# Kernel tuning notes

Hardware: AMD Instinct MI355X
Metric: run time of the kernel (lower is better)

The kernel has to match this reference:

```python
import jax, jax.numpy as jnp
import numpy as np

B, C, H, W = 16, 64, 128, 128
MX, MY = 24, 24
HIDDEN = max(1, int(C * 0.5))


def setup_inputs() -> dict:
    key = jax.random.key(0)
    ks = jax.random.split(key, 9)
    scale = 1.0 / (C * C)
    return {
        "x": jax.random.normal(ks[0], (B, C, H, W), jnp.float32),
        "w_real": scale * jax.random.normal(ks[1], (MX, MY, C, C), jnp.float32),
        "w_imag": scale * jax.random.normal(ks[2], (MX, MY, C, C), jnp.float32),
        "w_skip": jax.random.normal(ks[3], (C, C), jnp.float32) * (1.0 / np.sqrt(C)),
        "fc1_w": jax.random.normal(ks[4], (HIDDEN, C), jnp.float32) * (1.0 / np.sqrt(C)),
        "fc1_b": jnp.zeros((HIDDEN,), jnp.float32),
        "fc2_w": jax.random.normal(ks[5], (C, HIDDEN), jnp.float32) * (1.0 / np.sqrt(HIDDEN)),
        "fc2_b": jnp.zeros((C,), jnp.float32),
        "gate": jnp.ones((1, C, 1, 1), jnp.float32),
    }


def _spectral_conv(x, w_real, w_imag):
    # x: (B, C, H, W). Hermitian-symmetric 2-D spectral conv, matching torch path.
    b, c, h, w = x.shape
    mx = min(MX, h)
    my = min(MY, w // 2 + 1)
    x_ft = jnp.fft.rfftn(x, axes=(-2, -1))            # (B, C, H, W//2+1) complex
    weight = (w_real[:mx, :my] + 1j * w_imag[:mx, :my]).astype(jnp.complex64)
    out_sl = jnp.einsum('bcxy,xyco->boxy', x_ft[:, :, :mx, :my], weight)
    out_ft = jnp.zeros((b, c, h, w // 2 + 1), jnp.complex64).at[:, :, :mx, :my].set(out_sl)
    # enforce_hermitian_symmetry=True: ifft over leading spatial dim, zero imag
    # of DC / Nyquist columns, then irfft over last dim.
    out_ft = jnp.fft.ifft(out_ft, n=h, axis=-2)
    out_ft = out_ft.at[..., 0].set(out_ft[..., 0].real.astype(jnp.complex64))
    if w % 2 == 0:
        out_ft = out_ft.at[..., -1].set(out_ft[..., -1].real.astype(jnp.complex64))
    return jnp.fft.irfft(out_ft, n=w, axis=-1)


def reference(x, w_real, w_imag, w_skip, fc1_w, fc1_b, fc2_w, fc2_b, gate):
    # fno skip: 1x1 conv, no bias
    skip = jnp.einsum('bchw,oc->bohw', x, w_skip)
    h1 = jax.nn.gelu(_spectral_conv(x, w_real, w_imag) + skip, approximate=False)
    # channel MLP (Conv1d kernel=1 == per-pixel channel matmul)
    z = jnp.einsum('bchw,kc->bkhw', h1, fc1_w) + fc1_b[None, :, None, None]
    z = jax.nn.gelu(z, approximate=False)
    z = jnp.einsum('bkhw,ck->bchw', z, fc2_w) + fc2_b[None, :, None, None]
    # soft-gating skip
    return z + gate * h1
```

## Files before the change

kernel.cpp:

```cpp
#include <hip/hip_runtime.h>
#include <hip/hip_bf16.h>

#define BF __hip_bfloat16


typedef __attribute__((ext_vector_type(8))) short s8b;
typedef __attribute__((ext_vector_type(4))) float f32x4;

__device__ __forceinline__ float erf_fast(float x) {
    float ax = fabsf(x);
    float t  = 1.0f / (1.0f + 0.3275911f * ax);
    float p  = t * (0.254829592f + t * (-0.284496736f + t * (1.421413741f
             + t * (-1.453152027f + t * 1.061405429f))));
    float r  = 1.0f - p * __expf(-ax * ax);
    return copysignf(r, x);
}
__device__ __forceinline__ float geluf(float v) {
    return 0.5f * v * (1.0f + erf_fast(v * 0.7071067811865476f));
}
__device__ __forceinline__ float bf2f(BF v) { return __bfloat162float(v); }
__device__ __forceinline__ short f2bs(float f) {
    union { BF h; short s; } u; u.h = __float2bfloat16(f); return u.s;
}
__device__ __forceinline__ s8b ld8f(const float* __restrict__ p) {
    float4 a = *(const float4*)p;
    float4 b = *(const float4*)(p + 4);
    s8b r;
    r[0] = f2bs(a.x); r[1] = f2bs(a.y); r[2] = f2bs(a.z); r[3] = f2bs(a.w);
    r[4] = f2bs(b.x); r[5] = f2bs(b.y); r[6] = f2bs(b.z); r[7] = f2bs(b.w);
    return r;
}

__global__ __launch_bounds__(256) void k_tw(BF* __restrict__ gB1,
                                            BF* __restrict__ gB2) {
    int idx = blockIdx.x * 256 + threadIdx.x;
    if (idx < 6144) {
        int y = idx >> 7, v = idx & 127;
        int yy = (y < 24) ? y : y - 24;
        int r = (v * yy) & 127;
        float s, c; __sincosf((float)r * 0.04908738521234052f, &s, &c);
        gB1[idx] = __float2bfloat16(y < 24 ? c : -s);
    } else {
        int j = idx - 6144;
        int xp = j >> 8, k = j & 255;
        int u = k & 127, half = k >> 7;
        int x = (xp < 24) ? xp : xp - 24;
        int r = (u * x) & 127;
        float s, c; __sincosf((float)r * 0.04908738521234052f, &s, &c);
        float val = (xp < 24) ? (half ? s : c) : (half ? c : -s);
        gB2[j] = __float2bfloat16(val);
    }
}

__global__ __launch_bounds__(256) void k_fwd(const float* __restrict__ x,
                                             const BF* __restrict__ gB1,
                                             const BF* __restrict__ gB2,
                                             BF* __restrict__ XrB,
                                             BF* __restrict__ XiB) {
    __shared__ __align__(16) short Tl[48 * 136];

    const int tid  = threadIdx.x;
    const int bc   = blockIdx.x;
    const int lane = tid & 63;
    const int wv   = tid >> 6;
    const int lr   = lane & 15;
    const int lg   = lane >> 4;

    {
        const float* xb = x + ((size_t)bc << 14);
        s8b af[2][4];
        #pragma unroll
        for (int m = 0; m < 2; ++m) {
            const int u = wv * 32 + m * 16 + lr;
            #pragma unroll
            for (int s = 0; s < 4; ++s)
                af[m][s] = ld8f(xb + (size_t)u * 128 + s * 32 + lg * 8);
        }
        f32x4 acc[2][3];
        #pragma unroll
        for (int m = 0; m < 2; ++m)
            #pragma unroll
            for (int n = 0; n < 3; ++n)
                #pragma unroll
                for (int r = 0; r < 4; ++r) acc[m][n][r] = 0.f;
        #pragma unroll
        for (int s = 0; s < 4; ++s)
            #pragma unroll
            for (int n = 0; n < 3; ++n) {
                s8b bfr = *(const s8b*)((const short*)gB1 + (n * 16 + lr) * 128 + s * 32 + lg * 8);
                #pragma unroll
                for (int m = 0; m < 2; ++m)
                    acc[m][n] = __builtin_amdgcn_mfma_f32_16x16x32_bf16(af[m][s], bfr, acc[m][n], 0, 0, 0);
            }
        #pragma unroll
        for (int m = 0; m < 2; ++m) {
            const int u0 = wv * 32 + m * 16 + lg * 4;
            #pragma unroll
            for (int n = 0; n < 3; ++n) {
                short4 t;
                t.x = f2bs(acc[m][n][0]); t.y = f2bs(acc[m][n][1]);
                t.z = f2bs(acc[m][n][2]); t.w = f2bs(acc[m][n][3]);
                *(short4*)&Tl[(n * 16 + lr) * 136 + u0] = t;
            }
        }
    }
    __syncthreads();

    for (int j = wv; j < 6; j += 4) {
        const int m = j / 3, n = j % 3;
        const int y  = m * 16 + lr;
        const int r1 = (y < 24) ? y      : 0;
        const int r2 = (y < 24) ? y + 24 : 0;
        f32x4 acc = {0.f, 0.f, 0.f, 0.f};
        #pragma unroll
        for (int s = 0; s < 8; ++s) {
            s8b a = *(const s8b*)&Tl[((s < 4) ? r1 : r2) * 136 + (s & 3) * 32 + lg * 8];
            s8b b = *(const s8b*)((const short*)gB2 + (n * 16 + lr) * 256 + s * 32 + lg * 8);
            acc = __builtin_amdgcn_mfma_f32_16x16x32_bf16(a, b, acc, 0, 0, 0);
        }
        const int col = n * 16 + lr;
        const int xc  = (col < 24) ? col : col - 24;
        BF* dst = (col < 24) ? XrB : XiB;
        #pragma unroll
        for (int r = 0; r < 4; ++r) {
            const int yo = m * 16 + lg * 4 + r;
            if (yo < 24)
                dst[(size_t)(xc * 24 + yo) * 1024 + bc] = __float2bfloat16(acc[r]);
        }
    }
}

__global__ __launch_bounds__(256) void k_mix(const float* __restrict__ wr_g,
                                             const float* __restrict__ wi_g,
                                             const BF* __restrict__ XrB,
                                             const BF* __restrict__ XiB,
                                             BF* __restrict__ SrB,
                                             BF* __restrict__ SiB) {
    __shared__ __align__(16) short Br[64 * 136], Bi[64 * 136];
    const int tid  = threadIdx.x;
    const int xy   = blockIdx.x;
    const int lane = tid & 63;
    const int wv   = tid >> 6;
    const int lr   = lane & 15;
    const int lg   = lane >> 4;

    const float* wrp = wr_g + ((size_t)xy << 12);
    const float* wip = wi_g + ((size_t)xy << 12);
    for (int i = tid; i < 4096; i += 256) {
        int c = i >> 6, o = i & 63;
        float vr = wrp[i], vi = wip[i];
        short br = f2bs(vr), bi = f2bs(vi), nbi = f2bs(-vi);
        Br[o * 136 + c]      = br;
        Br[o * 136 + 64 + c] = nbi;
        Bi[o * 136 + c]      = bi;
        Bi[o * 136 + 64 + c] = br;
    }

    s8b az[4];
    {
        const short* xr = (const short*)XrB + ((size_t)xy << 10) + lr * 64;
        const short* xi = (const short*)XiB + ((size_t)xy << 10) + lr * 64;
        #pragma unroll
        for (int s = 0; s < 2; ++s) {
            az[s]     = *(const s8b*)(xr + s * 32 + lg * 8);
            az[s + 2] = *(const s8b*)(xi + s * 32 + lg * 8);
        }
    }
    __syncthreads();

    f32x4 ar = {0.f, 0.f, 0.f, 0.f}, ai = {0.f, 0.f, 0.f, 0.f};
    #pragma unroll
    for (int s = 0; s < 4; ++s) {
        s8b brf = *(const s8b*)&Br[(wv * 16 + lr) * 136 + s * 32 + lg * 8];
        ar = __builtin_amdgcn_mfma_f32_16x16x32_bf16(az[s], brf, ar, 0, 0, 0);
    }
    #pragma unroll
    for (int s = 0; s < 4; ++s) {
        s8b bif = *(const s8b*)&Bi[(wv * 16 + lr) * 136 + s * 32 + lg * 8];
        ai = __builtin_amdgcn_mfma_f32_16x16x32_bf16(az[s], bif, ai, 0, 0, 0);
    }

    const int o = wv * 16 + lr;
    #pragma unroll
    for (int r = 0; r < 4; ++r) {
        int b = lg * 4 + r;
        size_t base = (size_t)((b << 6) + o) * 576 + xy;
        SrB[base] = __float2bfloat16(ar[r]);
        SiB[base] = __float2bfloat16(ai[r]);
    }
}

__global__ __launch_bounds__(256) void k_invP(const BF* __restrict__ SrB,
                                              const BF* __restrict__ SiB,
                                              BF* __restrict__ PrB,
                                              BF* __restrict__ PiB) {
    __shared__ __align__(16) short Bp[48 * 72];
    const int tid  = threadIdx.x;
    const int bo   = blockIdx.x;
    const int lane = tid & 63;
    const int wv   = tid >> 6;
    const int lr   = lane & 15;
    const int lg   = lane >> 4;
    const float inv = 6.103515625e-05f;

    for (int i = tid; i < 576; i += 256) {
        int x = i / 24, y = i - x * 24;
        float sr = bf2f(SrB[(size_t)bo * 576 + i]);
        float si = bf2f(SiB[(size_t)bo * 576 + i]);
        float sc = (y == 0) ? inv : 2.0f * inv;
        Bp[y * 72 + x]             = f2bs(sc * sr);
        Bp[y * 72 + 24 + x]        = f2bs(-sc * si);
        Bp[(24 + y) * 72 + x]      = f2bs((y == 0) ? 0.f : sc * si);
        Bp[(24 + y) * 72 + 24 + x] = f2bs((y == 0) ? 0.f : sc * sr);
    }
    for (int i = tid; i < 768; i += 256)
        Bp[(i >> 4) * 72 + 48 + (i & 15)] = 0;

    s8b a[2][2];
    #pragma unroll
    for (int m = 0; m < 2; ++m) {
        const int u = wv * 32 + m * 16 + lr;
        #pragma unroll
        for (int s = 0; s < 2; ++s) {
            #pragma unroll
            for (int j = 0; j < 8; ++j) {
                const int k = s * 32 + lg * 8 + j;
                float val = 0.f;
                if (k < 48) {
                    int x = (k < 24) ? k : k - 24;
                    int r = (u * x) & 127;
                    float sn, cs;
                    __sincosf((float)r * 0.04908738521234052f, &sn, &cs);
                    val = (k < 24) ? cs : sn;
                }
                a[m][s][j] = f2bs(val);
            }
        }
    }
    __syncthreads();

    #pragma unroll
    for (int m = 0; m < 2; ++m)
        #pragma unroll
        for (int n = 0; n < 3; ++n) {
            f32x4 acc = {0.f, 0.f, 0.f, 0.f};
            #pragma unroll
            for (int s = 0; s < 2; ++s) {
                s8b bfr = *(const s8b*)&Bp[(n * 16 + lr) * 72 + s * 32 + lg * 8];
                acc = __builtin_amdgcn_mfma_f32_16x16x32_bf16(a[m][s], bfr, acc, 0, 0, 0);
            }
            const int col = n * 16 + lr;
            BF* dst = (col < 24) ? PrB : PiB;
            const int y = (col < 24) ? col : col - 24;
            #pragma unroll
            for (int r = 0; r < 4; ++r) {
                const int u = wv * 32 + m * 16 + lg * 4 + r;
                dst[(size_t)bo * 3072 + (size_t)u * 24 + y] = __float2bfloat16(acc[r]);
            }
        }
}

__global__ __launch_bounds__(256) void k_fused(const float* __restrict__ x,
                                               const BF* __restrict__ PrB,
                                               const BF* __restrict__ PiB,
                                               const float* __restrict__ wsk,
                                               const float* __restrict__ w1,
                                               const float* __restrict__ b1,
                                               const float* __restrict__ w2,
                                               const float* __restrict__ b2,
                                               const float* __restrict__ gt,
                                               float* __restrict__ out) {
    __shared__ __align__(16) short Plds[64 * 72];
    __shared__ __align__(16) short H1s[128 * 72];
    __shared__ __align__(16) short Zls[128 * 40];

    const int tid  = threadIdx.x;
    const int b    = blockIdx.x >> 7;
    const int u    = blockIdx.x & 127;
    const int lane = tid & 63;
    const int wv   = tid >> 6;
    const int lr   = lane & 15;
    const int lg   = lane >> 4;
    const int vb   = wv * 32;

    {
        const size_t pb = (size_t)(b * 64) * 3072 + (size_t)u * 24;
        for (int i = tid; i < 1536; i += 256) {
            int o = i / 24, y = i - o * 24;
            size_t g = pb + (size_t)o * 3072 + y;
            Plds[o * 72 + y]      = *(const short*)&PrB[g];
            Plds[o * 72 + 24 + y] = *(const short*)&PiB[g];
        }
        for (int i = tid; i < 1024; i += 256)
            Plds[(i >> 4) * 72 + 48 + (i & 15)] = 0;
    }

    s8b bx[2][2];
    {
        const float* xb = x + (size_t)(b * 64) * 16384 + (size_t)u * 128;
        #pragma unroll
        for (int nv = 0; nv < 2; ++nv) {
            const int v = vb + nv * 16 + lr;
            #pragma unroll
            for (int s = 0; s < 2; ++s)
                #pragma unroll
                for (int j = 0; j < 8; ++j)
                    bx[nv][s][j] = f2bs(xb[(size_t)(s * 32 + lg * 8 + j) * 16384 + v]);
        }
    }

    s8b btw[2][2];
    #pragma unroll
    for (int nv = 0; nv < 2; ++nv) {
        const int v = vb + nv * 16 + lr;
        #pragma unroll
        for (int s = 0; s < 2; ++s) {
            #pragma unroll
            for (int j = 0; j < 8; ++j) {
                const int k = s * 32 + lg * 8 + j;
                float val = 0.f;
                if (k < 24) {
                    int r = (v * k) & 127;
                    val = __cosf((float)r * 0.04908738521234052f);
                } else if (k < 48) {
                    int r = (v * (k - 24)) & 127;
                    val = -__sinf((float)r * 0.04908738521234052f);
                }
                btw[nv][s][j] = f2bs(val);
            }
        }
    }
    __syncthreads();

    f32x4 acc[4][2];
    #pragma unroll
    for (int mo = 0; mo < 4; ++mo)
        #pragma unroll
        for (int nv = 0; nv < 2; ++nv)
            #pragma unroll
            for (int r = 0; r < 4; ++r) acc[mo][nv][r] = 0.f;

    #pragma unroll
    for (int s = 0; s < 2; ++s)
        #pragma unroll
        for (int mo = 0; mo < 4; ++mo) {
            s8b ap = *(const s8b*)&Plds[(mo * 16 + lr) * 72 + s * 32 + lg * 8];
            #pragma unroll
            for (int nv = 0; nv < 2; ++nv)
                acc[mo][nv] = __builtin_amdgcn_mfma_f32_16x16x32_bf16(ap, btw[nv][s], acc[mo][nv], 0, 0, 0);
        }
    #pragma unroll
    for (int s = 0; s < 2; ++s)
        #pragma unroll
        for (int mo = 0; mo < 4; ++mo) {
            s8b aw = ld8f(wsk + (mo * 16 + lr) * 64 + s * 32 + lg * 8);
            #pragma unroll
            for (int nv = 0; nv < 2; ++nv)
                acc[mo][nv] = __builtin_amdgcn_mfma_f32_16x16x32_bf16(aw, bx[nv][s], acc[mo][nv], 0, 0, 0);
        }

    f32x4 h1r[4][2];
    #pragma unroll
    for (int mo = 0; mo < 4; ++mo)
        #pragma unroll
        for (int nv = 0; nv < 2; ++nv)
            #pragma unroll
            for (int r = 0; r < 4; ++r) {
                float h = geluf(acc[mo][nv][r]);
                h1r[mo][nv][r] = h;
                H1s[(vb + nv * 16 + lr) * 72 + mo * 16 + lg * 4 + r] = f2bs(h);
            }
    __syncthreads();

    f32x4 zac[2][2];
    #pragma unroll
    for (int mk = 0; mk < 2; ++mk)
        #pragma unroll
        for (int nv = 0; nv < 2; ++nv)
            #pragma unroll
            for (int r = 0; r < 4; ++r) zac[mk][nv][r] = 0.f;
    #pragma unroll
    for (int s = 0; s < 2; ++s) {
        s8b bh[2];
        #pragma unroll
        for (int nv = 0; nv < 2; ++nv)
            bh[nv] = *(const s8b*)&H1s[(vb + nv * 16 + lr) * 72 + s * 32 + lg * 8];
        #pragma unroll
        for (int mk = 0; mk < 2; ++mk) {
            s8b aw = ld8f(w1 + (mk * 16 + lr) * 64 + s * 32 + lg * 8);
            #pragma unroll
            for (int nv = 0; nv < 2; ++nv)
                zac[mk][nv] = __builtin_amdgcn_mfma_f32_16x16x32_bf16(aw, bh[nv], zac[mk][nv], 0, 0, 0);
        }
    }
    #pragma unroll
    for (int mk = 0; mk < 2; ++mk)
        #pragma unroll
        for (int r = 0; r < 4; ++r) {
            const float bb = b1[mk * 16 + lg * 4 + r];
            #pragma unroll
            for (int nv = 0; nv < 2; ++nv)
                Zls[(vb + nv * 16 + lr) * 40 + mk * 16 + lg * 4 + r] =
                    f2bs(geluf(zac[mk][nv][r] + bb));
        }
    __syncthreads();

    f32x4 oac[4][2];
    #pragma unroll
    for (int mo = 0; mo < 4; ++mo)
        #pragma unroll
        for (int nv = 0; nv < 2; ++nv)
            #pragma unroll
            for (int r = 0; r < 4; ++r) oac[mo][nv][r] = 0.f;
    s8b bz[2];
    #pragma unroll
    for (int nv = 0; nv < 2; ++nv)
        bz[nv] = *(const s8b*)&Zls[(vb + nv * 16 + lr) * 40 + lg * 8];
    #pragma unroll
    for (int mo = 0; mo < 4; ++mo) {
        s8b aw = ld8f(w2 + (mo * 16 + lr) * 32 + lg * 8);
        #pragma unroll
        for (int nv = 0; nv < 2; ++nv)
            oac[mo][nv] = __builtin_amdgcn_mfma_f32_16x16x32_bf16(aw, bz[nv], oac[mo][nv], 0, 0, 0);
    }

    float* ob = out + (size_t)(b * 64) * 16384 + (size_t)u * 128;
    #pragma unroll
    for (int mo = 0; mo < 4; ++mo)
        #pragma unroll
        for (int r = 0; r < 4; ++r) {
            const int o = mo * 16 + lg * 4 + r;
            const float b2v = b2[o];
            const float gv  = gt[o];
            #pragma unroll
            for (int nv = 0; nv < 2; ++nv)
                ob[(size_t)o * 16384 + vb + nv * 16 + lr] =
                    oac[mo][nv][r] + b2v + gv * h1r[mo][nv][r];
        }
}

extern "C" void kernel_launch(void* const* d_in, const int* in_sizes, int n_in,
                              void* d_out, int out_size, void* d_ws, size_t ws_size,
                              hipStream_t stream) {
    (void)in_sizes; (void)n_in; (void)out_size; (void)ws_size;
    const float* x   = (const float*)d_in[0];
    const float* wr  = (const float*)d_in[1];
    const float* wi  = (const float*)d_in[2];
    const float* wsk = (const float*)d_in[3];
    const float* w1  = (const float*)d_in[4];
    const float* b1  = (const float*)d_in[5];
    const float* w2  = (const float*)d_in[6];
    const float* b2  = (const float*)d_in[7];
    const float* gt  = (const float*)d_in[8];

    BF* wsB = (BF*)d_ws;
    BF* gB1 = wsB;
    BF* gB2 = wsB + 6144;
    BF* Xr  = wsB + 6291456;
    BF* Xi  = wsB + 6881280;
    BF* Sr  = wsB;
    BF* Si  = wsB + 589824;
    BF* Pr  = wsB + 1179648;
    BF* Pi  = wsB + 4325376;

    hipLaunchKernelGGL(k_tw,   dim3(72),   dim3(256), 0, stream, gB1, gB2);
    hipLaunchKernelGGL(k_fwd,  dim3(1024), dim3(256), 0, stream, x, gB1, gB2, Xr, Xi);
    hipLaunchKernelGGL(k_mix,  dim3(576),  dim3(256), 0, stream, wr, wi, Xr, Xi, Sr, Si);
    hipLaunchKernelGGL(k_invP, dim3(1024), dim3(256), 0, stream, Sr, Si, Pr, Pi);
    hipLaunchKernelGGL(k_fused, dim3(2048), dim3(256), 0, stream,
                       x, Pr, Pi, wsk, w1, b1, w2, b2, gt, (float*)d_out);
}
```

Before: 222.9 us.

## Precompute twiddle tables and bf16 weights once, shrink mix LDS and Pi storage

The setup kernel now also builds bf16 twiddle tables for the inverse-P and fused stages and converts the skip and MLP weights to bf16 once. k_invP and k_fused load these tables from memory instead of running sincos per lane, and load packed bf16 weights instead of converting fp32 on the fly. k_mix stores only the real and imaginary weights in half-size LDS and gets the negated term by flipping the sign bit of the activations. The always-zero first imaginary column of P is no longer stored, which cuts intermediate traffic. The cost is more workspace and extra global loads of the tables.

```diff
diff --git a/kernel.cpp b/kernel.cpp
--- a/kernel.cpp
+++ b/kernel.cpp
@@ -31,24 +31,56 @@
     return r;
 }
 
-__global__ __launch_bounds__(256) void k_tw(BF* __restrict__ gB1,
-                                            BF* __restrict__ gB2) {
-    int idx = blockIdx.x * 256 + threadIdx.x;
+__global__ __launch_bounds__(256) void k_tw(const float* __restrict__ wsk,
+                                            const float* __restrict__ w1,
+                                            const float* __restrict__ w2,
+                                            BF* __restrict__ gB1,
+                                            BF* __restrict__ gB2,
+                                            BF* __restrict__ gTw,
+                                            BF* __restrict__ gTa,
+                                            BF* __restrict__ wkB,
+                                            BF* __restrict__ w1B,
+                                            BF* __restrict__ w2B) {
+    const int idx = blockIdx.x * 256 + threadIdx.x;
+    const float th = 0.04908738521234052f;
     if (idx < 6144) {
         int y = idx >> 7, v = idx & 127;
         int yy = (y < 24) ? y : y - 24;
         int r = (v * yy) & 127;
-        float s, c; __sincosf((float)r * 0.04908738521234052f, &s, &c);
+        float s, c; __sincosf((float)r * th, &s, &c);
         gB1[idx] = __float2bfloat16(y < 24 ? c : -s);
-    } else {
+    } else if (idx < 18432) {
         int j = idx - 6144;
         int xp = j >> 8, k = j & 255;
         int u = k & 127, half = k >> 7;
         int x = (xp < 24) ? xp : xp - 24;
         int r = (u * x) & 127;
-        float s, c; __sincosf((float)r * 0.04908738521234052f, &s, &c);
+        float s, c; __sincosf((float)r * th, &s, &c);
         float val = (xp < 24) ? (half ? s : c) : (half ? c : -s);
         gB2[j] = __float2bfloat16(val);
+    } else if (idx < 26624) {
+        int j = idx - 18432;
+        int v = j >> 6, k = j & 63;
+        float val = 0.f;
+        if (k < 24)      val =  __cosf((float)((v * k) & 127) * th);
+        else if (k < 48) val = -__sinf((float)((v * (k - 24)) & 127) * th);
+        gTw[j] = __float2bfloat16(val);
+    } else if (idx < 34816) {
+        int j = idx - 26624;
+        int u = j >> 6, k = j & 63;
+        float val = 0.f;
+        if (k < 24)      val = __cosf((float)((u * k) & 127) * th);
+        else if (k < 48) val = __sinf((float)((u * (k - 24)) & 127) * th);
+        gTa[j] = __float2bfloat16(val);
+    } else if (idx < 38912) {
+        int j = idx - 34816;
+        wkB[j] = __float2bfloat16(wsk[j]);
+    } else if (idx < 40960) {
+        int j = idx - 38912;
+        w1B[j] = __float2bfloat16(w1[j]);
+    } else if (idx < 43008) {
+        int j = idx - 40960;
+        w2B[j] = __float2bfloat16(w2[j]);
     }
 }
 
@@ -136,7 +168,7 @@
                                              const BF* __restrict__ XiB,
                                              BF* __restrict__ SrB,
                                              BF* __restrict__ SiB) {
-    __shared__ __align__(16) short Br[64 * 136], Bi[64 * 136];
+    __shared__ __align__(16) short Br[64 * 72], Bi[64 * 72];
     const int tid  = threadIdx.x;
     const int xy   = blockIdx.x;
     const int lane = tid & 63;
@@ -148,36 +180,34 @@
     const float* wip = wi_g + ((size_t)xy << 12);
     for (int i = tid; i < 4096; i += 256) {
         int c = i >> 6, o = i & 63;
-        float vr = wrp[i], vi = wip[i];
-        short br = f2bs(vr), bi = f2bs(vi), nbi = f2bs(-vi);
-        Br[o * 136 + c]      = br;
-        Br[o * 136 + 64 + c] = nbi;
-        Bi[o * 136 + c]      = bi;
-        Bi[o * 136 + 64 + c] = br;
-    }
-
-    s8b az[4];
+        Br[o * 72 + c] = f2bs(wrp[i]);
+        Bi[o * 72 + c] = f2bs(wip[i]);
+    }
+
+    s8b axr[2], axi[2], axin[2];
     {
         const short* xr = (const short*)XrB + ((size_t)xy << 10) + lr * 64;
         const short* xi = (const short*)XiB + ((size_t)xy << 10) + lr * 64;
         #pragma unroll
         for (int s = 0; s < 2; ++s) {
-            az[s]     = *(const s8b*)(xr + s * 32 + lg * 8);
-            az[s + 2] = *(const s8b*)(xi + s * 32 + lg * 8);
+            axr[s] = *(const s8b*)(xr + s * 32 + lg * 8);
+            axi[s] = *(const s8b*)(xi + s * 32 + lg * 8);
+            #pragma unroll
+            for (int j = 0; j < 8; ++j)
+                axin[s][j] = axi[s][j] ^ (short)0x8000;
         }
     }
     __syncthreads();
 
     f32x4 ar = {0.f, 0.f, 0.f, 0.f}, ai = {0.f, 0.f, 0.f, 0.f};
     #pragma unroll
-    for (int s = 0; s < 4; ++s) {
-        s8b brf = *(const s8b*)&Br[(wv * 16 + lr) * 136 + s * 32 + lg * 8];
-        ar = __builtin_amdgcn_mfma_f32_16x16x32_bf16(az[s], brf, ar, 0, 0, 0);
-    }
-    #pragma unroll
-    for (int s = 0; s < 4; ++s) {
-        s8b bif = *(const s8b*)&Bi[(wv * 16 + lr) * 136 + s * 32 + lg * 8];
-        ai = __builtin_amdgcn_mfma_f32_16x16x32_bf16(az[s], bif, ai, 0, 0, 0);
+    for (int s = 0; s < 2; ++s) {
+        s8b wrf = *(const s8b*)&Br[(wv * 16 + lr) * 72 + s * 32 + lg * 8];
+        s8b wif = *(const s8b*)&Bi[(wv * 16 + lr) * 72 + s * 32 + lg * 8];
+        ar = __builtin_amdgcn_mfma_f32_16x16x32_bf16(axr[s],  wrf, ar, 0, 0, 0);
+        ar = __builtin_amdgcn_mfma_f32_16x16x32_bf16(axin[s], wif, ar, 0, 0, 0);
+        ai = __builtin_amdgcn_mfma_f32_16x16x32_bf16(axr[s],  wif, ai, 0, 0, 0);
+        ai = __builtin_amdgcn_mfma_f32_16x16x32_bf16(axi[s],  wrf, ai, 0, 0, 0);
     }
 
     const int o = wv * 16 + lr;
@@ -192,6 +222,7 @@
 
 __global__ __launch_bounds__(256) void k_invP(const BF* __restrict__ SrB,
                                               const BF* __restrict__ SiB,
+                                              const BF* __restrict__ gTa,
                                               BF* __restrict__ PrB,
                                               BF* __restrict__ PiB) {
     __shared__ __align__(16) short Bp[48 * 72];
@@ -217,24 +248,14 @@
         Bp[(i >> 4) * 72 + 48 + (i & 15)] = 0;
 
     s8b a[2][2];
-    #pragma unroll
-    for (int m = 0; m < 2; ++m) {
-        const int u = wv * 32 + m * 16 + lr;
-        #pragma unroll
-        for (int s = 0; s < 2; ++s) {
-            #pragma unroll
-            for (int j = 0; j < 8; ++j) {
-                const int k = s * 32 + lg * 8 + j;
-                float val = 0.f;
-                if (k < 48) {
-                    int x = (k < 24) ? k : k - 24;
-                    int r = (u * x) & 127;
-                    float sn, cs;
-                    __sincosf((float)r * 0.04908738521234052f, &sn, &cs);
-                    val = (k < 24) ? cs : sn;
-                }
-                a[m][s][j] = f2bs(val);
-            }
+    {
+        const short* gta = (const short*)gTa;
+        #pragma unroll
+        for (int m = 0; m < 2; ++m) {
+            const int u = wv * 32 + m * 16 + lr;
+            #pragma unroll
+            for (int s = 0; s < 2; ++s)
+                a[m][s] = *(const s8b*)&gta[u * 64 + s * 32 + lg * 8];
         }
     }
     __syncthreads();
@@ -250,12 +271,16 @@
                 acc = __builtin_amdgcn_mfma_f32_16x16x32_bf16(a[m][s], bfr, acc, 0, 0, 0);
             }
             const int col = n * 16 + lr;
-            BF* dst = (col < 24) ? PrB : PiB;
-            const int y = (col < 24) ? col : col - 24;
             #pragma unroll
             for (int r = 0; r < 4; ++r) {
                 const int u = wv * 32 + m * 16 + lg * 4 + r;
-                dst[(size_t)bo * 3072 + (size_t)u * 24 + y] = __float2bfloat16(acc[r]);
+                if (col < 24) {
+                    PrB[(size_t)bo * 3072 + (size_t)u * 24 + col] = __float2bfloat16(acc[r]);
+                } else {
+                    const int y = col - 24;
+                    if (y > 0)
+                        PiB[(size_t)bo * 2944 + (size_t)u * 23 + (y - 1)] = __float2bfloat16(acc[r]);
+                }
             }
         }
 }
@@ -263,10 +288,11 @@
 __global__ __launch_bounds__(256) void k_fused(const float* __restrict__ x,
                                                const BF* __restrict__ PrB,
                                                const BF* __restrict__ PiB,
-                                               const float* __restrict__ wsk,
-                                               const float* __restrict__ w1,
+                                               const BF* __restrict__ gTw,
+                                               const BF* __restrict__ wkB,
+                                               const BF* __restrict__ w1B,
+                                               const BF* __restrict__ w2B,
                                                const float* __restrict__ b1,
-                                               const float* __restrict__ w2,
                                                const float* __restrict__ b2,
                                                const float* __restrict__ gt,
                                                float* __restrict__ out) {
@@ -282,22 +308,23 @@
     const int lr   = lane & 15;
     const int lg   = lane >> 4;
     const int vb   = wv * 32;
-
-    {
-        const size_t pb = (size_t)(b * 64) * 3072 + (size_t)u * 24;
-        for (int i = tid; i < 1536; i += 256) {
-            int o = i / 24, y = i - o * 24;
-            size_t g = pb + (size_t)o * 3072 + y;
-            Plds[o * 72 + y]      = *(const short*)&PrB[g];
-            Plds[o * 72 + 24 + y] = *(const short*)&PiB[g];
-        }
-        for (int i = tid; i < 1024; i += 256)
-            Plds[(i >> 4) * 72 + 48 + (i & 15)] = 0;
-    }
+    const int b64  = b * 64;
+
+    for (int i = tid; i < 1536; i += 256) {
+        int o = i / 24, y = i - o * 24;
+        Plds[o * 72 + y] = *(const short*)&PrB[(size_t)(b64 + o) * 3072 + (size_t)u * 24 + y];
+    }
+    for (int i = tid; i < 1472; i += 256) {
+        int o = i / 23, y1 = i - o * 23;
+        Plds[o * 72 + 25 + y1] = *(const short*)&PiB[(size_t)(b64 + o) * 2944 + (size_t)u * 23 + y1];
+    }
+    if (tid < 64) Plds[tid * 72 + 24] = 0;
+    for (int i = tid; i < 1024; i += 256)
+        Plds[(i >> 4) * 72 + 48 + (i & 15)] = 0;
 
     s8b bx[2][2];
     {
-        const float* xb = x + (size_t)(b * 64) * 16384 + (size_t)u * 128;
+        const float* xb = x + (size_t)b64 * 16384 + (size_t)u * 128;
         #pragma unroll
         for (int nv = 0; nv < 2; ++nv) {
             const int v = vb + nv * 16 + lr;
@@ -310,27 +337,21 @@
     }
 
     s8b btw[2][2];
-    #pragma unroll
-    for (int nv = 0; nv < 2; ++nv) {
-        const int v = vb + nv * 16 + lr;
-        #pragma unroll
-        for (int s = 0; s < 2; ++s) {
-            #pragma unroll
-            for (int j = 0; j < 8; ++j) {
-                const int k = s * 32 + lg * 8 + j;
-                float val = 0.f;
-                if (k < 24) {
-                    int r = (v * k) & 127;
-                    val = __cosf((float)r * 0.04908738521234052f);
-                } else if (k < 48) {
-                    int r = (v * (k - 24)) & 127;
-                    val = -__sinf((float)r * 0.04908738521234052f);
-                }
-                btw[nv][s][j] = f2bs(val);
-            }
-        }
-    }
-    __syncthreads();
+    {
+        const short* gtw = (const short*)gTw;
+        #pragma unroll
+        for (int nv = 0; nv < 2; ++nv) {
+            const int v = vb + nv * 16 + lr;
+            #pragma unroll
+            for (int s = 0; s < 2; ++s)
+                btw[nv][s] = *(const s8b*)&gtw[v * 64 + s * 32 + lg * 8];
+        }
+    }
+    __syncthreads();
+
+    const short* wkb = (const short*)wkB;
+    const short* w1b = (const short*)w1B;
+    const short* w2b = (const short*)w2B;
 
     f32x4 acc[4][2];
     #pragma unroll
@@ -353,7 +374,7 @@
     for (int s = 0; s < 2; ++s)
         #pragma unroll
         for (int mo = 0; mo < 4; ++mo) {
-            s8b aw = ld8f(wsk + (mo * 16 + lr) * 64 + s * 32 + lg * 8);
+            s8b aw = *(const s8b*)&wkb[(mo * 16 + lr) * 64 + s * 32 + lg * 8];
             #pragma unroll
             for (int nv = 0; nv < 2; ++nv)
                 acc[mo][nv] = __builtin_amdgcn_mfma_f32_16x16x32_bf16(aw, bx[nv][s], acc[mo][nv], 0, 0, 0);
@@ -387,7 +408,7 @@
             bh[nv] = *(const s8b*)&H1s[(vb + nv * 16 + lr) * 72 + s * 32 + lg * 8];
         #pragma unroll
         for (int mk = 0; mk < 2; ++mk) {
-            s8b aw = ld8f(w1 + (mk * 16 + lr) * 64 + s * 32 + lg * 8);
+            s8b aw = *(const s8b*)&w1b[(mk * 16 + lr) * 64 + s * 32 + lg * 8];
             #pragma unroll
             for (int nv = 0; nv < 2; ++nv)
                 zac[mk][nv] = __builtin_amdgcn_mfma_f32_16x16x32_bf16(aw, bh[nv], zac[mk][nv], 0, 0, 0);
@@ -418,13 +439,13 @@
         bz[nv] = *(const s8b*)&Zls[(vb + nv * 16 + lr) * 40 + lg * 8];
     #pragma unroll
     for (int mo = 0; mo < 4; ++mo) {
-        s8b aw = ld8f(w2 + (mo * 16 + lr) * 32 + lg * 8);
+        s8b aw = *(const s8b*)&w2b[(mo * 16 + lr) * 32 + lg * 8];
         #pragma unroll
         for (int nv = 0; nv < 2; ++nv)
             oac[mo][nv] = __builtin_amdgcn_mfma_f32_16x16x32_bf16(aw, bz[nv], oac[mo][nv], 0, 0, 0);
     }
 
-    float* ob = out + (size_t)(b * 64) * 16384 + (size_t)u * 128;
+    float* ob = out + (size_t)b64 * 16384 + (size_t)u * 128;
     #pragma unroll
     for (int mo = 0; mo < 4; ++mo)
         #pragma unroll
@@ -456,17 +477,23 @@
     BF* wsB = (BF*)d_ws;
     BF* gB1 = wsB;
     BF* gB2 = wsB + 6144;
-    BF* Xr  = wsB + 6291456;
-    BF* Xi  = wsB + 6881280;
     BF* Sr  = wsB;
     BF* Si  = wsB + 589824;
     BF* Pr  = wsB + 1179648;
     BF* Pi  = wsB + 4325376;
-
-    hipLaunchKernelGGL(k_tw,   dim3(72),   dim3(256), 0, stream, gB1, gB2);
+    BF* Xr  = wsB + 6160384;
+    BF* Xi  = wsB + 6750208;
+    BF* gTw = wsB + 7340032;
+    BF* gTa = wsB + 7348224;
+    BF* wkB = wsB + 7356416;
+    BF* w1B = wsB + 7360512;
+    BF* w2B = wsB + 7362560;
+
+    hipLaunchKernelGGL(k_tw,   dim3(168),  dim3(256), 0, stream,
+                       wsk, w1, w2, gB1, gB2, gTw, gTa, wkB, w1B, w2B);
     hipLaunchKernelGGL(k_fwd,  dim3(1024), dim3(256), 0, stream, x, gB1, gB2, Xr, Xi);
     hipLaunchKernelGGL(k_mix,  dim3(576),  dim3(256), 0, stream, wr, wi, Xr, Xi, Sr, Si);
-    hipLaunchKernelGGL(k_invP, dim3(1024), dim3(256), 0, stream, Sr, Si, Pr, Pi);
+    hipLaunchKernelGGL(k_invP, dim3(1024), dim3(256), 0, stream, Sr, Si, gTa, Pr, Pi);
     hipLaunchKernelGGL(k_fused, dim3(2048), dim3(256), 0, stream,
-                       x, Pr, Pi, wsk, w1, b1, w2, b2, gt, (float*)d_out);
-}
+                       x, Pr, Pi, gTw, wkB, w1B, w2B, b1, b2, gt, (float*)d_out);
+}
```

Result: faster. 211.6 us (-5.1%).
